# Optimization experiments

Hardware: AMD Instinct MI355X
Metric: run time of the kernel (lower is better)

The kernel has to match this reference:

```python
import jax, jax.numpy as jnp
import numpy as np

N, D, K = 131072, 256, 8


def setup_inputs() -> dict:
    key = jax.random.key(0)
    k1, k2, k3, k4 = jax.random.split(key, 4)
    u_hidden = jax.random.normal(k1, (N, D), dtype=jnp.float32)
    v_hidden = jax.random.normal(k2, (N, D), dtype=jnp.float32)
    # stack of K per-type bilinear weights, scaled like a Glorot-ish init
    weights = jax.random.normal(k3, (K, D, D), dtype=jnp.float32) / np.sqrt(D).astype(np.float32)
    type_idx = jax.random.randint(k4, (N,), 0, K)
    return {"u_hidden": u_hidden, "v_hidden": v_hidden, "weights": weights, "type_idx": type_idx}


def reference(u_hidden, v_hidden, weights, type_idx):
    # Dropout is identity in eval mode (deterministic reference).
    # Original loop: for each weight W_k -> sum((u @ W_k) * v, axis=1), stacked to [N, K].
    scores = jnp.einsum('nd,kde,ne->nk', u_hidden, weights, v_hidden)  # [N, K]
    # gather the per-sample type's score (policy_grad=False path)
    sel = jnp.take_along_axis(scores, type_idx[:, None], axis=1)  # [N, 1]
    out = jax.nn.sigmoid(sel)  # act
    return out.squeeze()  # [N]
```

## Files before the change

### kernel.cpp

```cpp
#include <hip/hip_runtime.h>
#include <hip/hip_bf16.h>


#define N_SAMPLES 131072
#define DIM 256
#define KTYPES 8
#define TILE_M 64
#define MAXTILES (N_SAMPLES / TILE_M + KTYPES)

typedef _Float16 f16x8 __attribute__((ext_vector_type(8)));
typedef float f32x4 __attribute__((ext_vector_type(4)));

#define WT_OFF   ((size_t)0)
#define CNT_OFF  ((size_t)0x100000)
#define CUR_OFF  ((size_t)0x100020)
#define GOF_OFF  ((size_t)0x100040)
#define DESC_OFF ((size_t)0x100080)
#define PERM_OFF (DESC_OFF + (size_t)MAXTILES * 16)

__global__ void convw_kernel(const float* __restrict__ W, _Float16* __restrict__ Wt) {
    int g = blockIdx.x * 256 + threadIdx.x;
    int d  = g & 255;
    int e0 = ((g >> 8) & 63) * 4;
    int k  = g >> 14;
    const float* src = W + ((size_t)k << 16) + (size_t)d * 256 + e0;
    float4 vv = *(const float4*)src;
    _Float16* dst = Wt + ((size_t)k << 16) + d;
    dst[(size_t)(e0 + 0) * 256] = (_Float16)vv.x;
    dst[(size_t)(e0 + 1) * 256] = (_Float16)vv.y;
    dst[(size_t)(e0 + 2) * 256] = (_Float16)vv.z;
    dst[(size_t)(e0 + 3) * 256] = (_Float16)vv.w;
}

__global__ void hist_kernel(const int* __restrict__ idx, int* __restrict__ counts) {
    __shared__ int lcnt[KTYPES];
    if (threadIdx.x < KTYPES) lcnt[threadIdx.x] = 0;
    __syncthreads();
    int n = blockIdx.x * 256 + threadIdx.x;
    atomicAdd(&lcnt[idx[n]], 1);
    __syncthreads();
    if (threadIdx.x < KTYPES && lcnt[threadIdx.x] > 0)
        atomicAdd(&counts[threadIdx.x], lcnt[threadIdx.x]);
}

__global__ void plan_kernel(const int* __restrict__ counts, int* __restrict__ goff,
                            int4* __restrict__ desc) {
    __shared__ int s_goff[KTYPES + 1], s_tstart[KTYPES + 1], s_cnt[KTYPES];
    if (threadIdx.x == 0) {
        int off = 0, toff = 0;
        for (int k = 0; k < KTYPES; ++k) {
            int c = counts[k];
            s_cnt[k] = c;
            s_goff[k] = off; s_tstart[k] = toff;
            goff[k] = off;
            off += c;
            toff += (c + TILE_M - 1) / TILE_M;
        }
        s_goff[KTYPES] = off; s_tstart[KTYPES] = toff;
    }
    __syncthreads();
    int total = s_tstart[KTYPES];
    for (int t = threadIdx.x; t < MAXTILES; t += blockDim.x) {
        int4 dd;
        if (t < total) {
            int k = 0;
            while (t >= s_tstart[k + 1]) ++k;
            dd.x = k;
            dd.y = (t - s_tstart[k]) * TILE_M;
            dd.z = s_goff[k];
            dd.w = s_cnt[k];
        } else {
            dd = make_int4(-1, 0, 0, 0);
        }
        desc[t] = dd;
    }
}

__global__ void scatter_kernel(const int* __restrict__ idx, const int* __restrict__ goff,
                               int* __restrict__ cursors, int* __restrict__ perm) {
    __shared__ int lcnt[KTYPES], lbase[KTYPES];
    int tid = threadIdx.x;
    if (tid < KTYPES) lcnt[tid] = 0;
    __syncthreads();
    int n = blockIdx.x * 256 + tid;
    int k = idx[n];
    int lpos = atomicAdd(&lcnt[k], 1);
    __syncthreads();
    if (tid < KTYPES)
        lbase[tid] = (lcnt[tid] > 0) ? atomicAdd(&cursors[tid], lcnt[tid]) : 0;
    __syncthreads();
    perm[goff[k] + lbase[k] + lpos] = n;
}

__global__ __launch_bounds__(256, 4) void bilinear_main(
    const float* __restrict__ U, const float* __restrict__ V,
    const _Float16* __restrict__ Wt, const int* __restrict__ perm,
    const int4* __restrict__ desc, float* __restrict__ out)
{
    int4 dsc = desc[blockIdx.x];
    int k = dsc.x;
    if (k < 0) return;
    int local_base = dsc.y, goff = dsc.z, count = dsc.w;

    __shared__ __align__(16) _Float16 Wlds[32 * 256];

    int tid  = threadIdx.x;
    int wave = tid >> 6, lane = tid & 63;
    int lq = lane >> 4, lm = lane & 15;

    const _Float16* Wk = Wt + ((size_t)k << 16);

    int arow_local = wave * 16 + lm;
    bool avalid = (local_base + arow_local) < count;
    int an = perm[goff + local_base + (avalid ? arow_local : 0)];
    f16x8 afrag[8];
    {
        const float* up = U + ((size_t)an << 8) + lq * 8;
        #pragma unroll
        for (int ks = 0; ks < 8; ++ks) {
            float4 f0 = *(const float4*)(up + ks * 32);
            float4 f1 = *(const float4*)(up + ks * 32 + 4);
            f16x8 a;
            a[0] = (_Float16)f0.x; a[1] = (_Float16)f0.y;
            a[2] = (_Float16)f0.z; a[3] = (_Float16)f0.w;
            a[4] = (_Float16)f1.x; a[5] = (_Float16)f1.y;
            a[6] = (_Float16)f1.z; a[7] = (_Float16)f1.w;
            afrag[ks] = a;
        }
    }

    int vrow[4]; bool vvalid[4];
    #pragma unroll
    for (int r = 0; r < 4; ++r) {
        int rl = wave * 16 + lq * 4 + r;
        vvalid[r] = (local_base + rl) < count;
        vrow[r] = perm[goff + local_base + (vvalid[r] ? rl : 0)];
    }

    float spart[4] = {0.f, 0.f, 0.f, 0.f};

    for (int ec = 0; ec < 8; ++ec) {
        __syncthreads();
        #pragma unroll
        for (int it = 0; it < 4; ++it) {
            int elem = (it * 256 + tid) * 8;
            int e_l = elem >> 8, d0 = elem & 255;
            int byte = (e_l * 512 + d0 * 2) ^ ((e_l & 7) << 4);
            *(f16x8*)((char*)Wlds + byte) =
                *(const f16x8*)(Wk + (size_t)((ec * 32 + e_l) << 8) + d0);
        }
        __syncthreads();

        f32x4 acc0 = {0.f, 0.f, 0.f, 0.f};
        f32x4 acc1 = {0.f, 0.f, 0.f, 0.f};
        #pragma unroll
        for (int ks = 0; ks < 8; ++ks) {
            int dd = ks * 32 + lq * 8;
            int b0off = (lm * 512 + dd * 2) ^ ((lm & 7) << 4);
            int b1off = ((16 + lm) * 512 + dd * 2) ^ ((lm & 7) << 4);
            f16x8 b0 = *(const f16x8*)((char*)Wlds + b0off);
            f16x8 b1 = *(const f16x8*)((char*)Wlds + b1off);
            acc0 = __builtin_amdgcn_mfma_f32_16x16x32_f16(afrag[ks], b0, acc0, 0, 0, 0);
            acc1 = __builtin_amdgcn_mfma_f32_16x16x32_f16(afrag[ks], b1, acc1, 0, 0, 0);
        }
        #pragma unroll
        for (int r = 0; r < 4; ++r) {
            const float* vp = V + ((size_t)vrow[r] << 8) + ec * 32;
            spart[r] += acc0[r] * vp[lm] + acc1[r] * vp[16 + lm];
        }
    }

    #pragma unroll
    for (int r = 0; r < 4; ++r) {
        float s = spart[r];
        s += __shfl_xor(s, 1);
        s += __shfl_xor(s, 2);
        s += __shfl_xor(s, 4);
        s += __shfl_xor(s, 8);
        spart[r] = s;
    }
    if (lm < 4 && vvalid[lm]) {
        float s = spart[lm];
        out[vrow[lm]] = 1.0f / (1.0f + __expf(-s));
    }
}

extern "C" void kernel_launch(void* const* d_in, const int* in_sizes, int n_in,
                              void* d_out, int out_size, void* d_ws, size_t ws_size,
                              hipStream_t stream) {
    const float* U = (const float*)d_in[0];
    const float* V = (const float*)d_in[1];
    const float* W = (const float*)d_in[2];
    const int* idx = (const int*)d_in[3];
    float* out = (float*)d_out;
    char* ws = (char*)d_ws;

    _Float16* Wt  = (_Float16*)(ws + WT_OFF);
    int* counts   = (int*)(ws + CNT_OFF);
    int* cursors  = (int*)(ws + CUR_OFF);
    int* goff     = (int*)(ws + GOF_OFF);
    int4* desc    = (int4*)(ws + DESC_OFF);
    int* perm     = (int*)(ws + PERM_OFF);

    hipMemsetAsync(ws + CNT_OFF, 0, 64, stream);
    convw_kernel<<<512, 256, 0, stream>>>(W, Wt);
    hist_kernel<<<512, 256, 0, stream>>>(idx, counts);
    plan_kernel<<<1, 256, 0, stream>>>(counts, goff, desc);
    scatter_kernel<<<512, 256, 0, stream>>>(idx, goff, cursors, perm);
    bilinear_main<<<MAXTILES, 256, 0, stream>>>(U, V, Wt, perm, desc, out);
}
```

Before: 319.6 us.

## Load W fragments directly from global memory and merge prep kernels

```diff
diff --git a/kernel.cpp b/kernel.cpp
--- a/kernel.cpp
+++ b/kernel.cpp
@@ -18,26 +18,26 @@
 #define DESC_OFF ((size_t)0x100080)
 #define PERM_OFF (DESC_OFF + (size_t)MAXTILES * 16)
 
-__global__ void convw_kernel(const float* __restrict__ W, _Float16* __restrict__ Wt) {
-    int g = blockIdx.x * 256 + threadIdx.x;
-    int d  = g & 255;
-    int e0 = ((g >> 8) & 63) * 4;
-    int k  = g >> 14;
-    const float* src = W + ((size_t)k << 16) + (size_t)d * 256 + e0;
-    float4 vv = *(const float4*)src;
-    _Float16* dst = Wt + ((size_t)k << 16) + d;
-    dst[(size_t)(e0 + 0) * 256] = (_Float16)vv.x;
-    dst[(size_t)(e0 + 1) * 256] = (_Float16)vv.y;
-    dst[(size_t)(e0 + 2) * 256] = (_Float16)vv.z;
-    dst[(size_t)(e0 + 3) * 256] = (_Float16)vv.w;
-}
-
-__global__ void hist_kernel(const int* __restrict__ idx, int* __restrict__ counts) {
+__global__ void prep_kernel(const float* __restrict__ W, _Float16* __restrict__ Wt,
+                            const int* __restrict__ idx, int* __restrict__ counts) {
     __shared__ int lcnt[KTYPES];
     if (threadIdx.x < KTYPES) lcnt[threadIdx.x] = 0;
     __syncthreads();
-    int n = blockIdx.x * 256 + threadIdx.x;
-    atomicAdd(&lcnt[idx[n]], 1);
+
+    int g = blockIdx.x * 256 + threadIdx.x;
+    {
+        int d  = g & 255;
+        int e0 = ((g >> 8) & 63) * 4;
+        int k  = g >> 14;
+        const float* src = W + ((size_t)k << 16) + (size_t)d * 256 + e0;
+        float4 vv = *(const float4*)src;
+        _Float16* dst = Wt + ((size_t)k << 16) + d;
+        dst[(size_t)(e0 + 0) * 256] = (_Float16)vv.x;
+        dst[(size_t)(e0 + 1) * 256] = (_Float16)vv.y;
+        dst[(size_t)(e0 + 2) * 256] = (_Float16)vv.z;
+        dst[(size_t)(e0 + 3) * 256] = (_Float16)vv.w;
+    }
+    atomicAdd(&lcnt[idx[g]], 1);
     __syncthreads();
     if (threadIdx.x < KTYPES && lcnt[threadIdx.x] > 0)
         atomicAdd(&counts[threadIdx.x], lcnt[threadIdx.x]);
@@ -102,8 +102,6 @@
     if (k < 0) return;
     int local_base = dsc.y, goff = dsc.z, count = dsc.w;
 
-    __shared__ __align__(16) _Float16 Wlds[32 * 256];
-
     int tid  = threadIdx.x;
     int wave = tid >> 6, lane = tid & 63;
     int lq = lane >> 4, lm = lane & 15;
@@ -139,35 +137,29 @@
 
     float spart[4] = {0.f, 0.f, 0.f, 0.f};
 
+    #pragma unroll
     for (int ec = 0; ec < 8; ++ec) {
-        __syncthreads();
-        #pragma unroll
-        for (int it = 0; it < 4; ++it) {
-            int elem = (it * 256 + tid) * 8;
-            int e_l = elem >> 8, d0 = elem & 255;
-            int byte = (e_l * 512 + d0 * 2) ^ ((e_l & 7) << 4);
-            *(f16x8*)((char*)Wlds + byte) =
-                *(const f16x8*)(Wk + (size_t)((ec * 32 + e_l) << 8) + d0);
-        }
-        __syncthreads();
+        float va0[4], va1[4];
+        #pragma unroll
+        for (int r = 0; r < 4; ++r) {
+            const float* vp = V + ((size_t)vrow[r] << 8) + ec * 32;
+            va0[r] = vp[lm];
+            va1[r] = vp[16 + lm];
+        }
 
         f32x4 acc0 = {0.f, 0.f, 0.f, 0.f};
         f32x4 acc1 = {0.f, 0.f, 0.f, 0.f};
+        const _Float16* be0 = Wk + (size_t)((ec * 32 + lm) << 8) + lq * 8;
         #pragma unroll
         for (int ks = 0; ks < 8; ++ks) {
-            int dd = ks * 32 + lq * 8;
-            int b0off = (lm * 512 + dd * 2) ^ ((lm & 7) << 4);
-            int b1off = ((16 + lm) * 512 + dd * 2) ^ ((lm & 7) << 4);
-            f16x8 b0 = *(const f16x8*)((char*)Wlds + b0off);
-            f16x8 b1 = *(const f16x8*)((char*)Wlds + b1off);
+            f16x8 b0 = *(const f16x8*)(be0 + ks * 32);
+            f16x8 b1 = *(const f16x8*)(be0 + 16 * 256 + ks * 32);
             acc0 = __builtin_amdgcn_mfma_f32_16x16x32_f16(afrag[ks], b0, acc0, 0, 0, 0);
             acc1 = __builtin_amdgcn_mfma_f32_16x16x32_f16(afrag[ks], b1, acc1, 0, 0, 0);
         }
         #pragma unroll
-        for (int r = 0; r < 4; ++r) {
-            const float* vp = V + ((size_t)vrow[r] << 8) + ec * 32;
-            spart[r] += acc0[r] * vp[lm] + acc1[r] * vp[16 + lm];
-        }
+        for (int r = 0; r < 4; ++r)
+            spart[r] += acc0[r] * va0[r] + acc1[r] * va1[r];
     }
 
     #pragma unroll
@@ -203,8 +195,7 @@
     int* perm     = (int*)(ws + PERM_OFF);
 
     hipMemsetAsync(ws + CNT_OFF, 0, 64, stream);
-    convw_kernel<<<512, 256, 0, stream>>>(W, Wt);
-    hist_kernel<<<512, 256, 0, stream>>>(idx, counts);
+    prep_kernel<<<512, 256, 0, stream>>>(W, Wt, idx, counts);
     plan_kernel<<<1, 256, 0, stream>>>(counts, goff, desc);
     scatter_kernel<<<512, 256, 0, stream>>>(idx, goff, cursors, perm);
     bilinear_main<<<MAXTILES, 256, 0, stream>>>(U, V, Wt, perm, desc, out);
```

Result: slower. 418.9 us (+31.1%).
